# Optimization experiments

Measured on AMD Instinct MI355X. Metric: run time of the kernel, lower is better.

## Reference

```python
import jax, jax.numpy as jnp
import numpy as np

B, L_IN, D_MODEL, CONV_D, KSIZE = 16, 512, 384, 1536, 3
MEL_MAX = 4096
LN_EPS = 1e-5


def _conv1d_same(h, w, b):
    # h: [B, C_in, L], w: [C_out, C_in, K] -> [B, C_out, L]
    y = jax.lax.conv_general_dilated(h, w, window_strides=(1,), padding='SAME',
                                     dimension_numbers=('NCH', 'OIH', 'NCH'))
    return y + b[None, :, None]


def _layernorm(x, g, b):
    m = jnp.mean(x, -1, keepdims=True)
    v = jnp.mean((x - m) ** 2, -1, keepdims=True)
    return (x - m) * jax.lax.rsqrt(v + LN_EPS) * g + b


def _ffn(x, wa, ba, wb, bb):
    # Conv1D_FFT: conv(d_model->conv_d) ReLU conv(conv_d->d_model) ReLU
    h = jnp.transpose(x, (0, 2, 1))
    h = jax.nn.relu(_conv1d_same(h, wa, ba))
    h = jax.nn.relu(_conv1d_same(h, wb, bb))
    return jnp.transpose(h, (0, 2, 1))


def _dur_pred(x, w1, b1, w2, b2, g1, be1, w3, b3, w4, b4, g2, be2, wl, bl):
    h = _ffn(x, w1, b1, w2, b2)
    h = _layernorm(h, g1, be1)  # dropout is identity at eval
    h = _ffn(h, w3, b3, w4, b4)
    h = _layernorm(h, g2, be2)
    return (h @ wl + bl)[..., 0]  # [B, L_in], squeeze(-1)


def _length_regulate(x, dur, mel_max_len):
    # Equivalent to alignment @ x where alignment[b,t,j]=1 iff cum[b,j-1] <= t < cum[b,j],
    # padded with zeros out to mel_max_len (original pads output to mel_max_len).
    cum = jnp.cumsum(dur, axis=-1)                        # [B, L_in]
    total = cum[:, -1]                                    # [B]
    t = jnp.arange(mel_max_len, dtype=cum.dtype)          # [T]
    idx = jax.vmap(lambda c: jnp.searchsorted(c, t, side='right'))(cum)  # [B, T]
    idx = jnp.minimum(idx, x.shape[1] - 1)
    out = jnp.take_along_axis(x, idx[:, :, None], axis=1)  # [B, T, D]
    mask = (t[None, :] < total[:, None])[..., None]
    return out * mask


def setup_inputs() -> dict:
    key = jax.random.key(0)
    ks = jax.random.split(key, 8)
    def nrm(k, shape):
        return jax.random.normal(k, shape, jnp.float32) * 0.02
    return {
        'x': jax.random.normal(ks[0], (B, L_IN, D_MODEL), jnp.float32),
        'target': jax.random.randint(ks[1], (B, L_IN), 0, 8, jnp.int32),
        'mel_max_len': MEL_MAX,
        'w1': nrm(ks[2], (CONV_D, D_MODEL, KSIZE)), 'b1': jnp.zeros((CONV_D,), jnp.float32),
        'w2': nrm(ks[3], (D_MODEL, CONV_D, KSIZE)), 'b2': jnp.zeros((D_MODEL,), jnp.float32),
        'g1': jnp.ones((D_MODEL,), jnp.float32), 'be1': jnp.zeros((D_MODEL,), jnp.float32),
        'w3': nrm(ks[4], (CONV_D, D_MODEL, KSIZE)), 'b3': jnp.zeros((CONV_D,), jnp.float32),
        'w4': nrm(ks[5], (D_MODEL, CONV_D, KSIZE)), 'b4': jnp.zeros((D_MODEL,), jnp.float32),
        'g2': jnp.ones((D_MODEL,), jnp.float32), 'be2': jnp.zeros((D_MODEL,), jnp.float32),
        'wl': nrm(ks[6], (D_MODEL, 1)), 'bl': jnp.zeros((1,), jnp.float32),
    }


def reference(x, target, mel_max_len, w1, b1, w2, b2, g1, be1, w3, b3, w4, b4, g2, be2, wl, bl):
    dur_preds = _dur_pred(x, w1, b1, w2, b2, g1, be1, w3, b3, w4, b4, g2, be2, wl, bl)
    output = _length_regulate(x, target, mel_max_len)
    return (output, dur_preds)
```

## Files before the change

kernel.cpp:

```cpp
#include <hip/hip_runtime.h>
#include <hip/hip_bf16.h>
#include <cstddef>
#include <cstdint>

#define NB 16
#define LIN 512
#define DM 384
#define DC 1536
#define MELMAX 4096
#define LN_EPS 1e-5f

typedef __bf16 bf16x8 __attribute__((ext_vector_type(8)));
typedef float f32x4 __attribute__((ext_vector_type(4)));

#define GL2LDS(gp, lp)                                                                \
    __builtin_amdgcn_global_load_lds((const __attribute__((address_space(1))) void*)(gp), \
                                     (__attribute__((address_space(3))) void*)(lp), 16, 0, 0)

__device__ __forceinline__ float wred(float v) {
#pragma unroll
    for (int m = 32; m >= 1; m >>= 1) v += __shfl_xor(v, m, 64);
    return v;
}

__device__ __forceinline__ unsigned short f2bf(float f) {
    __hip_bfloat16 h = __float2bfloat16(f);
    return *reinterpret_cast<unsigned short*>(&h);
}

__device__ __forceinline__ float bf2f(unsigned short u) {
    return __uint_as_float(((unsigned)u) << 16);
}


__global__ void cumsum_kernel(const int* __restrict__ tgt, int* __restrict__ cum) {
    __shared__ int s[LIN];
    const int b = blockIdx.x, tid = threadIdx.x;
    s[tid] = tgt[b * LIN + tid];
    __syncthreads();
    for (int off = 1; off < LIN; off <<= 1) {
        int v = (tid >= off) ? s[tid - off] : 0;
        __syncthreads();
        s[tid] += v;
        __syncthreads();
    }
    cum[b * LIN + tid] = s[tid];
}


#define ZPAD_BLKS 96
#define CASTX_BLKS 3072
#define WCAST_BLKS 2304

__global__ void prep_kernel(const float* __restrict__ x, unsigned short* __restrict__ xb,
                            unsigned short* __restrict__ hbig, unsigned short* __restrict__ h2b,
                            const float* __restrict__ w1, const float* __restrict__ w2,
                            const float* __restrict__ w3, const float* __restrict__ w4,
                            unsigned short* __restrict__ o1, unsigned short* __restrict__ o2,
                            unsigned short* __restrict__ o3, unsigned short* __restrict__ o4) {
    const int bid = blockIdx.x, tid = threadIdx.x;
    if (bid < ZPAD_BLKS) {
        const int buf = bid >> 5, rem = bid & 31;
        const int b = rem >> 1, row = (rem & 1) ? (LIN + 1) : 0;
        unsigned short* p = buf == 0 ? xb : (buf == 1 ? hbig : h2b);
        const int rl = buf == 1 ? DC : DM;
        unsigned short* base = p + ((size_t)b * (LIN + 2) + row) * rl;
        for (int c = tid; c < rl; c += 256) base[c] = 0;
        return;
    }
    if (bid < ZPAD_BLKS + CASTX_BLKS) {
        const int idx = (bid - ZPAD_BLKS) * 256 + tid;
        const float4 v = reinterpret_cast<const float4*>(x)[idx];
        const int e = idx * 4;
        const int b = e / (LIN * DM);
        const int rem = e - b * (LIN * DM);
        const int l = rem / DM;
        const int c = rem - l * DM;
        ushort4 o;
        o.x = f2bf(v.x); o.y = f2bf(v.y); o.z = f2bf(v.z); o.w = f2bf(v.w);
        *reinterpret_cast<ushort4*>(xb + ((size_t)b * (LIN + 2) + l + 1) * DM + c) = o;
        return;
    }
    const int j = bid - ZPAD_BLKS - CASTX_BLKS;
    const int which = j / WCAST_BLKS;
    const int idx = (j - which * WCAST_BLKS) * 256 + tid;
    const float* w = which == 0 ? w1 : which == 1 ? w2 : which == 2 ? w3 : w4;
    unsigned short* gg = which == 0 ? o1 : which == 1 ? o2 : which == 2 ? o3 : o4;
    const int CI = (which == 0 || which == 2) ? DM : DC;
    const int co = idx / CI, ci = idx - co * CI;
    const float* p = w + (size_t)idx * 3;
    unsigned short* o = gg + (size_t)co * (3 * CI) + ci;
    o[0 * CI] = f2bf(p[0]);
    o[1 * CI] = f2bf(p[1]);
    o[2 * CI] = f2bf(p[2]);
}


template <int CI, int CO, int BN, bool FUSE>
__global__ __launch_bounds__(256, 2) void conv_mfma_kernel(const unsigned short* __restrict__ in,
                                                           const unsigned short* __restrict__ wg,
                                                           const float* __restrict__ bias,
                                                           unsigned short* __restrict__ out,
                                                           const float* __restrict__ xf,
                                                           const int* __restrict__ cum,
                                                           float* __restrict__ gout) {
    constexpr int BM = 128, BK = 32;
    constexpr int KC = CI / BK;
    constexpr int AROWS = BM + 16;
    constexpr int AGRP = AROWS / 16;
    constexpr int GPT = BN / 16;
    constexpr int BGRP = 3 * GPT;
    constexpr int NW_N = BN / 32;
    constexpr int NT = CO / BN;
    constexpr int NGB = FUSE ? 256 : 0;
    constexpr int NCONV = NB * (LIN / BM) * NT;

    __shared__ __align__(16) unsigned short As[2][AROWS * BK];
    __shared__ __align__(16) unsigned short Bs[2][3 * BN * BK];

    const int tid = threadIdx.x;
    const int lane = tid & 63;
    const int wv = tid >> 6;

    if (FUSE && blockIdx.x < NGB) {
        const int w0 = blockIdx.x * 4 + wv;
        for (int row = w0; row < NB * MELMAX; row += NGB * 4) {
            const int b = row >> 12;
            const int t = row & (MELMAX - 1);
            const int* c = cum + b * LIN;
            const int total = c[LIN - 1];
            float4* orow = reinterpret_cast<float4*>(gout + ((size_t)b * MELMAX + t) * DM);
            if (t < total) {
                int lo = 0, hi = LIN;
                while (lo < hi) { int mid = (lo + hi) >> 1; if (c[mid] > t) hi = mid; else lo = mid + 1; }
                const int idx = lo < (LIN - 1) ? lo : (LIN - 1);
                const float4* xrow = reinterpret_cast<const float4*>(xf + ((size_t)b * LIN + idx) * DM);
#pragma unroll
                for (int j = 0; j < 2; ++j) {
                    const int p = lane + 64 * j;
                    if (p < DM / 4) orow[p] = xrow[p];
                }
            } else {
                const float4 z = make_float4(0.f, 0.f, 0.f, 0.f);
#pragma unroll
                for (int j = 0; j < 2; ++j) {
                    const int p = lane + 64 * j;
                    if (p < DM / 4) orow[p] = z;
                }
            }
        }
        return;
    }

    const int orig = blockIdx.x - NGB;
    const int q = NCONV >> 3, xcd = orig & 7, o = orig >> 3;
    const int wgid = xcd * q + o;

    const int mg = wgid / NT;
    const int nt = wgid - mg * NT;
    const int b = mg >> 2;
    const int l0 = (mg & 3) * BM;
    const int n0 = nt * BN;

    const int wr = wv >> 1, wc = wv & 1;

    const unsigned short* inb = in + (size_t)b * (LIN + 2) * CI;

    f32x4 acc[4][NW_N];
#pragma unroll
    for (int m = 0; m < 4; ++m)
#pragma unroll
        for (int n = 0; n < NW_N; ++n) acc[m][n] = (f32x4){0.f, 0.f, 0.f, 0.f};

    const int lrow = lane >> 2;
    const int lch = lane & 3;
    const int fr = lane & 15, kg = lane >> 4;

    const unsigned short* aroot = inb + (size_t)l0 * CI + lch * 8;
    const unsigned short* broot = wg + (size_t)n0 * (3 * CI) + lch * 8;

#define STAGE(c, kb)                                                                      \
    do {                                                                                  \
        const unsigned short* abase = aroot + (kb) * BK;                                  \
        for (int g = wv; g < AGRP; g += 4)                                                \
            GL2LDS(abase + (size_t)(g * 16 + lrow) * CI, &As[c][g * 512]);                \
        const unsigned short* bbase = broot + (kb) * BK;                                  \
        for (int g2 = wv; g2 < BGRP; g2 += 4) {                                           \
            const int t = g2 / GPT, gr = g2 - t * GPT;                                    \
            GL2LDS(bbase + (size_t)(gr * 16 + lrow) * (3 * CI) + (size_t)t * CI,          \
                   &Bs[c][g2 * 512]);                                                     \
        }                                                                                 \
    } while (0)

#define COMPUTE(c)                                                                        \
    do {                                                                                  \
        _Pragma("unroll")                                                                 \
        for (int t = 0; t < 3; ++t) {                                                     \
            bf16x8 aF[4], bF[NW_N];                                                       \
            _Pragma("unroll")                                                             \
            for (int m = 0; m < 4; ++m)                                                   \
                aF[m] = *reinterpret_cast<const bf16x8*>(                                 \
                    &As[c][(t + wr * 64 + m * 16 + fr) * BK + kg * 8]);                   \
            _Pragma("unroll")                                                             \
            for (int n = 0; n < NW_N; ++n)                                                \
                bF[n] = *reinterpret_cast<const bf16x8*>(                                 \
                    &Bs[c][(t * BN + wc * (BN / 2) + n * 16 + fr) * BK + kg * 8]);        \
            _Pragma("unroll")                                                             \
            for (int m = 0; m < 4; ++m)                                                   \
                _Pragma("unroll")                                                         \
                for (int n = 0; n < NW_N; ++n)                                            \
                    acc[m][n] =                                                           \
                        __builtin_amdgcn_mfma_f32_16x16x32_bf16(aF[m], bF[n], acc[m][n],  \
                                                                0, 0, 0);                 \
        }                                                                                 \
    } while (0)

    STAGE(0, 0);
    __syncthreads();
#pragma unroll 1
    for (int kb = 0; kb < KC; kb += 2) {
        if (kb + 1 < KC) STAGE(1, kb + 1);
        COMPUTE(0);
        __syncthreads();
        if (kb + 2 < KC) STAGE(0, kb + 2);
        if (kb + 1 < KC) {
            COMPUTE(1);
            __syncthreads();
        }
    }
#undef STAGE
#undef COMPUTE

    const int fq = lane >> 4;
    float bv[NW_N];
#pragma unroll
    for (int n = 0; n < NW_N; ++n) bv[n] = bias[n0 + wc * (BN / 2) + n * 16 + fr];
    unsigned short* outb = out + (size_t)b * (LIN + 2) * CO;
#pragma unroll
    for (int m = 0; m < 4; ++m)
#pragma unroll
        for (int qy = 0; qy < 4; ++qy) {
            const int grow = l0 + wr * 64 + m * 16 + fq * 4 + qy + 1;
            unsigned short* orow = outb + (size_t)grow * CO + n0 + wc * (BN / 2) + fr;
#pragma unroll
            for (int n = 0; n < NW_N; ++n) {
                const float v = fmaxf(acc[m][n][qy] + bv[n], 0.f);
                orow[n * 16] = f2bf(v);
            }
        }
}


__global__ void ln_kernel(unsigned short* __restrict__ h, const float* __restrict__ g,
                          const float* __restrict__ be) {
    const int row = blockIdx.x, lane = threadIdx.x;
    const int b = row >> 9, l = row & (LIN - 1);
    unsigned short* hr = h + ((size_t)b * (LIN + 2) + l + 1) * DM;
    float v[6];
    float s = 0.f;
#pragma unroll
    for (int j = 0; j < 6; ++j) { v[j] = bf2f(hr[lane + 64 * j]); s += v[j]; }
    s = wred(s);
    const float mean = s * (1.f / DM);
    float vs = 0.f;
#pragma unroll
    for (int j = 0; j < 6; ++j) { const float d = v[j] - mean; vs += d * d; }
    vs = wred(vs);
    const float rstd = rsqrtf(vs * (1.f / DM) + LN_EPS);
#pragma unroll
    for (int j = 0; j < 6; ++j) {
        const int c = lane + 64 * j;
        hr[c] = f2bf((v[j] - mean) * rstd * g[c] + be[c]);
    }
}


__global__ void ln_linear_kernel(const unsigned short* __restrict__ h, const float* __restrict__ g,
                                 const float* __restrict__ be, const float* __restrict__ wl,
                                 const float* __restrict__ bl, float* __restrict__ dur) {
    const int row = blockIdx.x, lane = threadIdx.x;
    const int b = row >> 9, l = row & (LIN - 1);
    const unsigned short* hr = h + ((size_t)b * (LIN + 2) + l + 1) * DM;
    float v[6];
    float s = 0.f;
#pragma unroll
    for (int j = 0; j < 6; ++j) { v[j] = bf2f(hr[lane + 64 * j]); s += v[j]; }
    s = wred(s);
    const float mean = s * (1.f / DM);
    float vs = 0.f;
#pragma unroll
    for (int j = 0; j < 6; ++j) { const float d = v[j] - mean; vs += d * d; }
    vs = wred(vs);
    const float rstd = rsqrtf(vs * (1.f / DM) + LN_EPS);
    float dot = 0.f;
#pragma unroll
    for (int j = 0; j < 6; ++j) {
        const int c = lane + 64 * j;
        dot += ((v[j] - mean) * rstd * g[c] + be[c]) * wl[c];
    }
    dot = wred(dot);
    if (lane == 0) dur[row] = dot + bl[0];
}


extern "C" void kernel_launch(void* const* d_in, const int* in_sizes, int n_in,
                              void* d_out, int out_size, void* d_ws, size_t ws_size,
                              hipStream_t stream) {
    const float* x   = (const float*)d_in[0];
    const int*   tgt = (const int*)d_in[1];
    const float* w1  = (const float*)d_in[3];
    const float* b1  = (const float*)d_in[4];
    const float* w2  = (const float*)d_in[5];
    const float* b2  = (const float*)d_in[6];
    const float* g1  = (const float*)d_in[7];
    const float* be1 = (const float*)d_in[8];
    const float* w3  = (const float*)d_in[9];
    const float* b3  = (const float*)d_in[10];
    const float* w4  = (const float*)d_in[11];
    const float* b4  = (const float*)d_in[12];
    const float* g2  = (const float*)d_in[13];
    const float* be2 = (const float*)d_in[14];
    const float* wl  = (const float*)d_in[15];
    const float* bl  = (const float*)d_in[16];

    float* out = (float*)d_out;
    float* dur = out + (size_t)NB * MELMAX * DM;

    unsigned short* ws = (unsigned short*)d_ws;
    unsigned short* xb   = ws;
    unsigned short* hbig = xb + (size_t)NB * (LIN + 2) * DM;
    unsigned short* h2b  = hbig + (size_t)NB * (LIN + 2) * DC;
    unsigned short* wg1  = h2b + (size_t)NB * (LIN + 2) * DM;
    unsigned short* wg2  = wg1 + (size_t)DC * 3 * DM;
    unsigned short* wg3  = wg2 + (size_t)DM * 3 * DC;
    unsigned short* wg4  = wg3 + (size_t)DC * 3 * DM;
    int* cum = (int*)(wg4 + (size_t)DM * 3 * DC);

    cumsum_kernel<<<NB, LIN, 0, stream>>>(tgt, cum);
    prep_kernel<<<ZPAD_BLKS + CASTX_BLKS + 4 * WCAST_BLKS, 256, 0, stream>>>(
        x, xb, hbig, h2b, w1, w2, w3, w4, wg1, wg2, wg3, wg4);

    const int NCONV1 = NB * (LIN / 128) * (DC / 128);
    conv_mfma_kernel<DM, DC, 128, true><<<256 + NCONV1, 256, 0, stream>>>(
        xb, wg1, b1, hbig, x, cum, out);

    conv_mfma_kernel<DC, DM, 64, false><<<NB * (LIN / 128) * (DM / 64), 256, 0, stream>>>(
        hbig, wg2, b2, h2b, nullptr, nullptr, nullptr);
    ln_kernel<<<NB * LIN, 64, 0, stream>>>(h2b, g1, be1);
    conv_mfma_kernel<DM, DC, 128, false><<<NB * (LIN / 128) * (DC / 128), 256, 0, stream>>>(
        h2b, wg3, b3, hbig, nullptr, nullptr, nullptr);
    conv_mfma_kernel<DC, DM, 64, false><<<NB * (LIN / 128) * (DM / 64), 256, 0, stream>>>(
        hbig, wg4, b4, xb, nullptr, nullptr, nullptr);
    ln_linear_kernel<<<NB * LIN, 64, 0, stream>>>(xb, g2, be2, wl, bl, dur);
}
```

Before: 246.2 us.

## Unfuse gather into standalone kernel and pipeline conv loads with vmcnt waits

Result: faster. 223.9 us (-9.1%).

```diff
diff --git a/kernel.cpp b/kernel.cpp
--- a/kernel.cpp
+++ b/kernel.cpp
@@ -45,6 +45,37 @@
         __syncthreads();
     }
     cum[b * LIN + tid] = s[tid];
+}
+
+
+__global__ __launch_bounds__(256) void gather_kernel(const float* __restrict__ x,
+                                                     const int* __restrict__ cum,
+                                                     float* __restrict__ out) {
+    const int wid = (blockIdx.x * 256 + threadIdx.x) >> 6;
+    const int lane = threadIdx.x & 63;
+    const int b = wid >> 12;
+    const int t = wid & (MELMAX - 1);
+    const int* c = cum + b * LIN;
+    const int total = c[LIN - 1];
+    float4* orow = reinterpret_cast<float4*>(out + ((size_t)b * MELMAX + t) * DM);
+    if (t < total) {
+        int lo = 0, hi = LIN;
+        while (lo < hi) { int mid = (lo + hi) >> 1; if (c[mid] > t) hi = mid; else lo = mid + 1; }
+        const int idx = lo < (LIN - 1) ? lo : (LIN - 1);
+        const float4* xrow = reinterpret_cast<const float4*>(x + ((size_t)b * LIN + idx) * DM);
+#pragma unroll
+        for (int j = 0; j < 2; ++j) {
+            const int p = lane + 64 * j;
+            if (p < DM / 4) orow[p] = xrow[p];
+        }
+    } else {
+        const float4 z = make_float4(0.f, 0.f, 0.f, 0.f);
+#pragma unroll
+        for (int j = 0; j < 2; ++j) {
+            const int p = lane + 64 * j;
+            if (p < DM / 4) orow[p] = z;
+        }
+    }
 }
 
 
@@ -96,63 +127,28 @@
 }
 
 
-template <int CI, int CO, int BN, bool FUSE>
+template <int CI, int CO, int BN>
 __global__ __launch_bounds__(256, 2) void conv_mfma_kernel(const unsigned short* __restrict__ in,
                                                            const unsigned short* __restrict__ wg,
                                                            const float* __restrict__ bias,
-                                                           unsigned short* __restrict__ out,
-                                                           const float* __restrict__ xf,
-                                                           const int* __restrict__ cum,
-                                                           float* __restrict__ gout) {
+                                                           unsigned short* __restrict__ out) {
     constexpr int BM = 128, BK = 32;
     constexpr int KC = CI / BK;
-    constexpr int AROWS = BM + 16;
-    constexpr int AGRP = AROWS / 16;
+    constexpr int AGRP = 12;
     constexpr int GPT = BN / 16;
     constexpr int BGRP = 3 * GPT;
     constexpr int NW_N = BN / 32;
     constexpr int NT = CO / BN;
-    constexpr int NGB = FUSE ? 256 : 0;
     constexpr int NCONV = NB * (LIN / BM) * NT;
 
-    __shared__ __align__(16) unsigned short As[2][AROWS * BK];
-    __shared__ __align__(16) unsigned short Bs[2][3 * BN * BK];
+    __shared__ __align__(16) unsigned short As[2][AGRP * 512];
+    __shared__ __align__(16) unsigned short Bs[2][BGRP * 512];
 
     const int tid = threadIdx.x;
     const int lane = tid & 63;
     const int wv = tid >> 6;
 
-    if (FUSE && blockIdx.x < NGB) {
-        const int w0 = blockIdx.x * 4 + wv;
-        for (int row = w0; row < NB * MELMAX; row += NGB * 4) {
-            const int b = row >> 12;
-            const int t = row & (MELMAX - 1);
-            const int* c = cum + b * LIN;
-            const int total = c[LIN - 1];
-            float4* orow = reinterpret_cast<float4*>(gout + ((size_t)b * MELMAX + t) * DM);
-            if (t < total) {
-                int lo = 0, hi = LIN;
-                while (lo < hi) { int mid = (lo + hi) >> 1; if (c[mid] > t) hi = mid; else lo = mid + 1; }
-                const int idx = lo < (LIN - 1) ? lo : (LIN - 1);
-                const float4* xrow = reinterpret_cast<const float4*>(xf + ((size_t)b * LIN + idx) * DM);
-#pragma unroll
-                for (int j = 0; j < 2; ++j) {
-                    const int p = lane + 64 * j;
-                    if (p < DM / 4) orow[p] = xrow[p];
-                }
-            } else {
-                const float4 z = make_float4(0.f, 0.f, 0.f, 0.f);
-#pragma unroll
-                for (int j = 0; j < 2; ++j) {
-                    const int p = lane + 64 * j;
-                    if (p < DM / 4) orow[p] = z;
-                }
-            }
-        }
-        return;
-    }
-
-    const int orig = blockIdx.x - NGB;
+    const int orig = blockIdx.x;
     const int q = NCONV >> 3, xcd = orig & 7, o = orig >> 3;
     const int wgid = xcd * q + o;
 
@@ -182,9 +178,13 @@
 #define STAGE(c, kb)                                                                      \
     do {                                                                                  \
         const unsigned short* abase = aroot + (kb) * BK;                                  \
-        for (int g = wv; g < AGRP; g += 4)                                                \
-            GL2LDS(abase + (size_t)(g * 16 + lrow) * CI, &As[c][g * 512]);                \
+        _Pragma("unroll")                                                                 \
+        for (int g = wv; g < AGRP; g += 4) {                                              \
+            const int sg = g < 9 ? g : 0;    \
+            GL2LDS(abase + (size_t)(sg * 16 + lrow) * CI, &As[c][g * 512]);               \
+        }                                                                                 \
         const unsigned short* bbase = broot + (kb) * BK;                                  \
+        _Pragma("unroll")                                                                 \
         for (int g2 = wv; g2 < BGRP; g2 += 4) {                                           \
             const int t = g2 / GPT, gr = g2 - t * GPT;                                    \
             GL2LDS(bbase + (size_t)(gr * 16 + lrow) * (3 * CI) + (size_t)t * CI,          \
@@ -216,17 +216,25 @@
     } while (0)
 
     STAGE(0, 0);
-    __syncthreads();
+    STAGE(1, 1);
 #pragma unroll 1
-    for (int kb = 0; kb < KC; kb += 2) {
-        if (kb + 1 < KC) STAGE(1, kb + 1);
-        COMPUTE(0);
-        __syncthreads();
-        if (kb + 2 < KC) STAGE(0, kb + 2);
-        if (kb + 1 < KC) {
-            COMPUTE(1);
-            __syncthreads();
-        }
+    for (int kb = 0; kb < KC; ++kb) {
+        const int cur = kb & 1;
+        if constexpr (BN == 128)
+            asm volatile("s_waitcnt vmcnt(9)" ::: "memory");
+        else
+            asm volatile("s_waitcnt vmcnt(6)" ::: "memory");
+        __builtin_amdgcn_sched_barrier(0);
+        __builtin_amdgcn_s_barrier();
+        __builtin_amdgcn_sched_barrier(0);
+        COMPUTE(cur);
+        asm volatile("s_waitcnt lgkmcnt(0)" ::: "memory");
+        __builtin_amdgcn_sched_barrier(0);
+        __builtin_amdgcn_s_barrier();
+        __builtin_amdgcn_sched_barrier(0);
+        int nk = kb + 2;
+        if (nk >= KC) nk -= KC;
+        STAGE(cur, nk);
     }
 #undef STAGE
 #undef COMPUTE
@@ -337,19 +345,15 @@
     int* cum = (int*)(wg4 + (size_t)DM * 3 * DC);
 
     cumsum_kernel<<<NB, LIN, 0, stream>>>(tgt, cum);
+    gather_kernel<<<(NB * MELMAX) / 4, 256, 0, stream>>>(x, cum, out);
+
     prep_kernel<<<ZPAD_BLKS + CASTX_BLKS + 4 * WCAST_BLKS, 256, 0, stream>>>(
         x, xb, hbig, h2b, w1, w2, w3, w4, wg1, wg2, wg3, wg4);
 
-    const int NCONV1 = NB * (LIN / 128) * (DC / 128);
-    conv_mfma_kernel<DM, DC, 128, true><<<256 + NCONV1, 256, 0, stream>>>(
-        xb, wg1, b1, hbig, x, cum, out);
-
-    conv_mfma_kernel<DC, DM, 64, false><<<NB * (LIN / 128) * (DM / 64), 256, 0, stream>>>(
-        hbig, wg2, b2, h2b, nullptr, nullptr, nullptr);
+    conv_mfma_kernel<DM, DC, 128><<<NB * (LIN / 128) * (DC / 128), 256, 0, stream>>>(xb, wg1, b1, hbig);
+    conv_mfma_kernel<DC, DM, 64><<<NB * (LIN / 128) * (DM / 64), 256, 0, stream>>>(hbig, wg2, b2, h2b);
     ln_kernel<<<NB * LIN, 64, 0, stream>>>(h2b, g1, be1);
-    conv_mfma_kernel<DM, DC, 128, false><<<NB * (LIN / 128) * (DC / 128), 256, 0, stream>>>(
-        h2b, wg3, b3, hbig, nullptr, nullptr, nullptr);
-    conv_mfma_kernel<DC, DM, 64, false><<<NB * (LIN / 128) * (DM / 64), 256, 0, stream>>>(
-        hbig, wg4, b4, xb, nullptr, nullptr, nullptr);
+    conv_mfma_kernel<DM, DC, 128><<<NB * (LIN / 128) * (DC / 128), 256, 0, stream>>>(h2b, wg3, b3, hbig);
+    conv_mfma_kernel<DC, DM, 64><<<NB * (LIN / 128) * (DM / 64), 256, 0, stream>>>(hbig, wg4, b4, xb);
     ln_linear_kernel<<<NB * LIN, 64, 0, stream>>>(xb, g2, be2, wl, bl, dur);
 }
```
